# Kernel optimization log

Hardware: AMD Instinct MI355X
Metric: run time of the kernel (lower is better)

Reference implementation:

```python
import jax, jax.numpy as jnp
import numpy as np

B, S, D, H, L, V, NP, GH = 2, 1024, 1024, 16, 6, 32000, 16, 64
DH = D // H
FF = int(D * 4 * 2 / 3)  # SwiGLU hidden = int(dim*ffn_expansion*2/3)


def setup_inputs() -> dict:
    key = jax.random.key(0)
    ks = jax.random.split(key, 12)
    n = lambda k, shp, s=0.02: (jax.random.normal(k, shp, jnp.float32) * s)
    # per-layer memory gate init: -3.0 .. -1.0 across layers
    gate_init = jnp.array([-3.0 + (i / (L - 1)) * 2.0 for i in range(L)], jnp.float32)
    return dict(
        input_ids=jax.random.randint(ks[0], (B, S), 0, V),
        tok_emb=n(ks[1], (V, D)),
        w_init=jnp.zeros((D,), jnp.float32),
        persistent=n(ks[2], (NP, D), 1.0),
        norm1_w=jnp.ones((L, D), jnp.float32),
        norm2_w=jnp.ones((L, D), jnp.float32),
        norm_f_w=jnp.ones((D,), jnp.float32),
        qkv_w=n(ks[3], (L, 3 * D, D)),
        q_norm_w=jnp.ones((L, DH), jnp.float32),
        k_norm_w=jnp.ones((L, DH), jnp.float32),
        gamma_w1=n(ks[4], (L, GH, D)),
        gamma_w2=n(ks[5], (L, 1, GH)),
        memory_gate=gate_init,
        w_o=n(ks[6], (L, D, D), 0.02 / 2 ** 0.5),
        ffn_w1=n(ks[7], (L, FF, D)),
        ffn_w2=n(ks[8], (L, FF, D)),
        ffn_w3=n(ks[9], (L, D, FF)),
    )


def _rms(x, w, eps=1e-6):
    return x * jax.lax.rsqrt(jnp.mean(x * x, axis=-1, keepdims=True) + eps) * w


def _rope_tables():
    inv_freq = 1.0 / (10000.0 ** (jnp.arange(0, DH, 2, dtype=jnp.float32) / DH))
    t = jnp.arange(S, dtype=jnp.float32)
    freqs = jnp.einsum('s,f->sf', t, inv_freq)  # (S, DH/2)
    return jnp.cos(freqs), jnp.sin(freqs)


def _rope(x, cos, sin):  # x: (B,H,S,DH)
    x1, x2 = jnp.split(x, 2, axis=-1)
    return jnp.concatenate([x1 * cos - x2 * sin, x2 * cos + x1 * sin], axis=-1)


def reference(input_ids, tok_emb, w_init, persistent, norm1_w, norm2_w, norm_f_w,
              qkv_w, q_norm_w, k_norm_w, gamma_w1, gamma_w2, memory_gate,
              w_o, ffn_w1, ffn_w2, ffn_w3):
    x = tok_emb[input_ids] + w_init  # (B,S,D)
    cos, sin = _rope_tables()
    causal = jnp.tril(jnp.ones((S, S), dtype=bool))  # True where k <= q
    scale = DH ** -0.5
    # persistent memory: per-head sum of key outer products M_p[h] = sum_j p_jh p_jh^T
    p = persistent.reshape(NP, H, DH)
    Mp = jnp.einsum('nhd,nhe->hde', p, p)
    for i in range(L):
        h = _rms(x, norm1_w[i])
        qkv = h @ qkv_w[i].T  # (B,S,3D)
        q, k, v = jnp.split(qkv, 3, axis=-1)
        q = q.reshape(B, S, H, DH).transpose(0, 2, 1, 3)
        k = k.reshape(B, S, H, DH).transpose(0, 2, 1, 3)
        v = v.reshape(B, S, H, DH).transpose(0, 2, 1, 3)
        q = _rms(q, q_norm_w[i])  # qk_norm
        k = _rms(k, k_norm_w[i])
        q = _rope(q, cos, sin)
        k = _rope(k, cos, sin)
        # gamma gate: Linear -> SiLU -> Linear -> Sigmoid, (B,S,1)
        g = jax.nn.sigmoid(jnp.einsum('oh,bsh->bso', gamma_w2[i],
                                      jax.nn.silu(jnp.einsum('hd,bsd->bsh', gamma_w1[i], h))))
        gk = g[..., 0]  # (B,S)
        # Omega-rule memory: q'_t = (M_p q_t + sum_{i<=t} gamma_i (k_i . q_t) k_i) / (NP + sum_{i<=t} gamma_i)
        mem_scores = jnp.einsum('bhqd,bhkd->bhqk', q, k) * gk[:, None, None, :]
        mem_scores = jnp.where(causal, mem_scores, 0.0)
        mem = jnp.einsum('bhqk,bhkd->bhqd', mem_scores, k)
        mpq = jnp.einsum('hde,bhse->bhsd', Mp, q)
        norm = NP + jnp.cumsum(gk, axis=1)  # (B,S)
        q_proj = (mpq + mem) / norm[:, None, :, None]
        gate = jax.nn.sigmoid(memory_gate[i])
        q = (1 - gate) * q + gate * q_proj
        # causal softmax attention
        attn = jnp.einsum('bhqd,bhkd->bhqk', q, k) * scale
        attn = jnp.where(causal, attn, jnp.finfo(attn.dtype).min)
        pw = jax.nn.softmax(attn, axis=-1)
        o = jnp.einsum('bhqk,bhkd->bhqd', pw, v).transpose(0, 2, 1, 3).reshape(B, S, D)
        x = x + o @ w_o[i].T
        # SwiGLU FFN
        h2 = _rms(x, norm2_w[i])
        x = x + (jax.nn.silu(h2 @ ffn_w1[i].T) * (h2 @ ffn_w2[i].T)) @ ffn_w3[i].T
    x = _rms(x, norm_f_w)
    return x @ tok_emb.T  # tied lm_head, (B,S,V)
```

## Files before the change

kernel.cpp:

```cpp
#include <hip/hip_runtime.h>
#include <hip/hip_bf16.h>
#include <math.h>

#define B 2
#define S 1024
#define D 1024
#define H 16
#define DH 64
#define NL 6
#define GH 64
#define NP 16
#define V 32000
#define FF 2730
#define FFP 2752
#define M (B*S)

typedef float fv4 __attribute__((ext_vector_type(4)));
typedef short bf16x8 __attribute__((ext_vector_type(8)));
typedef unsigned short us4 __attribute__((ext_vector_type(4)));
typedef unsigned short us;

#define MFMA16 __builtin_amdgcn_mfma_f32_16x16x32_bf16
#define G2L16(g, l) __builtin_amdgcn_global_load_lds( \
    (const __attribute__((address_space(1))) void*)(g), \
    (__attribute__((address_space(3))) void*)(l), 16, 0, 0)

__device__ __forceinline__ us f2bf(float f) {
  union { float f; unsigned u; } v; v.f = f;
  unsigned r = v.u + 0x7FFFu + ((v.u >> 16) & 1u);
  return (us)(r >> 16);
}
__device__ __forceinline__ float bf2f(us h) {
  union { unsigned u; float f; } v; v.u = ((unsigned)h) << 16;
  return v.f;
}

template<int N> __device__ __forceinline__ void waitcnt_vm() {
  if constexpr (N == 0)      asm volatile("s_waitcnt vmcnt(0)" ::: "memory");
  else if constexpr (N == 4) asm volatile("s_waitcnt vmcnt(4)" ::: "memory");
  else if constexpr (N == 8) asm volatile("s_waitcnt vmcnt(8)" ::: "memory");
  else if constexpr (N == 6) asm volatile("s_waitcnt vmcnt(6)" ::: "memory");
}

__device__ __forceinline__ int xcd_remap(int flat, int nwg) {
  int q = nwg >> 3, r = nwg & 7;
  int xcd = flat & 7, idx = flat >> 3;
  return (xcd < r) ? (xcd * (q + 1) + idx) : (r * (q + 1) + (xcd - r) * q + idx);
}

__global__ __launch_bounds__(256) void k_embed(const int* __restrict__ ids,
                                               const float* __restrict__ emb,
                                               const float* __restrict__ winit,
                                               float* __restrict__ x) {
  int m = blockIdx.x, t = threadIdx.x;
  int id = ids[m];
  fv4 a = *(const fv4*)(emb + (size_t)id * D + 4*t);
  fv4 w = *(const fv4*)(winit + 4*t);
  *(fv4*)(x + (size_t)m * D + 4*t) = a + w;
}

__global__ void k_rope_tables(float* __restrict__ cosT, float* __restrict__ sinT) {
  int idx = blockIdx.x * blockDim.x + threadIdx.x;
  if (idx >= S * 32) return;
  int s = idx >> 5, f = idx & 31;
  float inv = powf(10000.0f, -2.0f * (float)f / (float)DH);
  float ang = (float)s * inv;
  cosT[idx] = cosf(ang);
  sinT[idx] = sinf(ang);
}

__global__ __launch_bounds__(256) void k_mp(const float* __restrict__ pers,
                                            us* __restrict__ Mp) {
  int h = blockIdx.x, t = threadIdx.x;
  __shared__ float p[NP][DH];
  for (int i = t; i < NP * DH; i += 256) {
    int n = i / DH, dh = i % DH;
    p[n][dh] = pers[(size_t)n * D + h * DH + dh];
  }
  __syncthreads();
  for (int i = t; i < DH * DH; i += 256) {
    int d = i / DH, e = i % DH;
    float s = 0.f;
#pragma unroll
    for (int n = 0; n < NP; n++) s += p[n][d] * p[n][e];
    Mp[(size_t)h * DH * DH + i] = f2bf(s);
  }
}

__global__ __launch_bounds__(256) void k_rms(const float* __restrict__ in,
                                             const float* __restrict__ w,
                                             us* __restrict__ outb) {
  int m = blockIdx.x, t = threadIdx.x;
  fv4 v = *(const fv4*)(in + (size_t)m * D + 4*t);
  float ss = v[0]*v[0] + v[1]*v[1] + v[2]*v[2] + v[3]*v[3];
#pragma unroll
  for (int off = 32; off > 0; off >>= 1) ss += __shfl_down(ss, off);
  __shared__ float buf[4];
  if ((t & 63) == 0) buf[t >> 6] = ss;
  __syncthreads();
  float tot = buf[0] + buf[1] + buf[2] + buf[3];
  float r = rsqrtf(tot * (1.0f / (float)D) + 1e-6f);
  fv4 wv = *(const fv4*)(w + 4*t);
  fv4 res = v * r * wv;
  us4 o; o[0]=f2bf(res[0]); o[1]=f2bf(res[1]); o[2]=f2bf(res[2]); o[3]=f2bf(res[3]);
  *(us4*)(outb + (size_t)m * D + 4*t) = o;
}

__global__ __launch_bounds__(256) void k_rmsg(const float* __restrict__ in,
                                              const float* __restrict__ w,
                                              const float* __restrict__ w1,
                                              const float* __restrict__ w2,
                                              us* __restrict__ outb,
                                              float* __restrict__ gko) {
  int m = blockIdx.x, t = threadIdx.x;
  __shared__ float hrow[D];
  __shared__ float buf[4];
  __shared__ float part[4][64];
  fv4 v = *(const fv4*)(in + (size_t)m * D + 4*t);
  float ss = v[0]*v[0] + v[1]*v[1] + v[2]*v[2] + v[3]*v[3];
#pragma unroll
  for (int off = 32; off > 0; off >>= 1) ss += __shfl_down(ss, off);
  if ((t & 63) == 0) buf[t >> 6] = ss;
  __syncthreads();
  float tot = buf[0] + buf[1] + buf[2] + buf[3];
  float r = rsqrtf(tot * (1.0f / (float)D) + 1e-6f);
  fv4 wv = *(const fv4*)(w + 4*t);
  fv4 res = v * r * wv;
  us4 o; o[0]=f2bf(res[0]); o[1]=f2bf(res[1]); o[2]=f2bf(res[2]); o[3]=f2bf(res[3]);
  *(us4*)(outb + (size_t)m * D + 4*t) = o;
  *(fv4*)&hrow[4*t] = res;
  __syncthreads();
  int oo = t & 63, seg = t >> 6;
  const float* wr = w1 + (size_t)oo * D + seg * 256;
  const float* hr = hrow + seg * 256;
  float acc = 0.f;
  for (int j = 0; j < 256; j += 4) {
    fv4 wv4 = *(const fv4*)(wr + j);
    acc += wv4[0]*hr[j] + wv4[1]*hr[j+1] + wv4[2]*hr[j+2] + wv4[3]*hr[j+3];
  }
  part[seg][oo] = acc;
  __syncthreads();
  if (t < 64) {
    float dot = part[0][t] + part[1][t] + part[2][t] + part[3][t];
    float sv = dot / (1.f + expf(-dot));
    float val = sv * w2[t];
#pragma unroll
    for (int off = 32; off > 0; off >>= 1) val += __shfl_down(val, off);
    if (t == 0) gko[m] = 1.f / (1.f + expf(-val));
  }
}

__global__ __launch_bounds__(256) void k_cvt(const float* __restrict__ src,
                                             us* __restrict__ dst, int n) {
  for (size_t i = ((size_t)blockIdx.x * 256 + threadIdx.x) * 4; i < (size_t)n;
       i += (size_t)gridDim.x * 1024) {
    fv4 v = *(const fv4*)(src + i);
    us4 o; o[0]=f2bf(v[0]); o[1]=f2bf(v[1]); o[2]=f2bf(v[2]); o[3]=f2bf(v[3]);
    *(us4*)(dst + i) = o;
  }
}

#define CVT_N1 786432
#define CVT_N2 262144
#define CVT_N3 698880
#define CVT_N4 698880
#define CVT_N5 704512
__global__ __launch_bounds__(256) void k_cvtw(const float* __restrict__ s1,
                                              const float* __restrict__ s2,
                                              const float* __restrict__ s3,
                                              const float* __restrict__ s4,
                                              const float* __restrict__ s5,
                                              us* __restrict__ d1, us* __restrict__ d2,
                                              us* __restrict__ d3, us* __restrict__ d4,
                                              us* __restrict__ d5) {
  const int TOT = CVT_N1 + CVT_N2 + CVT_N3 + CVT_N4 + CVT_N5;
  for (int i = blockIdx.x * 256 + threadIdx.x; i < TOT; i += gridDim.x * 256) {
    const float* s; us* d; int j = i;
    if (j < CVT_N1) { s = s1; d = d1; }
    else if ((j -= CVT_N1) < CVT_N2) { s = s2; d = d2; }
    else if ((j -= CVT_N2) < CVT_N3) { s = s3; d = d3; }
    else if ((j -= CVT_N3) < CVT_N4) { s = s4; d = d4; }
    else {
      j -= CVT_N4;
      int r = j / (FFP/4), c = (j % (FFP/4)) * 4;
      us4 o;
#pragma unroll
      for (int q = 0; q < 4; q++) {
        int cc = c + q;
        o[q] = (cc < FF) ? f2bf(s5[(size_t)r * FF + cc]) : (us)0;
      }
      *(us4*)&d5[(size_t)r * FFP + c] = o;
      continue;
    }
    fv4 v = *(const fv4*)(s + (size_t)4 * j);
    us4 o; o[0]=f2bf(v[0]); o[1]=f2bf(v[1]); o[2]=f2bf(v[2]); o[3]=f2bf(v[3]);
    *(us4*)&d[(size_t)4 * j] = o;
  }
}

template<int ACW, int BCW>
__device__ __forceinline__ void pg_stage(const us* __restrict__ A,
                                         const us* __restrict__ W,
                                         us* bufA, us* bufB,
                                         int m0, int n0, int Nn, int Kk,
                                         int tile, int w, int lane, int lr, int sx) {
#pragma unroll
  for (int i = 0; i < ACW; i++) {
    int chunk = w * ACW + i;
    G2L16(A + (size_t)(m0 + chunk*8 + lr) * Kk + tile*64 + sx, bufA + chunk*512 + lane*8);
  }
#pragma unroll
  for (int i = 0; i < BCW; i++) {
    int chunk = w * BCW + i;
    int wrow = n0 + chunk*8 + lr;
    if (wrow >= Nn) wrow = Nn - 1;
    G2L16(W + (size_t)wrow * Kk + tile*64 + sx, bufB + chunk*512 + lane*8);
  }
}

template<int EPI, int BM, int BN>
__global__ __launch_bounds__(256) void k_pgemm(const us* __restrict__ A,
                                               const us* __restrict__ W,
                                               float* __restrict__ C,
                                               int Nn, int Kk) {
  constexpr int FM = BM / 32, FN = BN / 32;
  constexpr int ACW = BM / 32, BCW = BN / 32;
  constexpr int L = ACW + BCW;
  __shared__ __attribute__((aligned(16))) us lds[2][(BM + BN) * 64];
  int t = threadIdx.x, lane = t & 63, w = t >> 6;
  int l16 = lane & 15, lkb = lane >> 4, lr = lane >> 3;
  int sx = ((lane & 7) ^ lr) * 8;
  int sw = l16 & 7;
  int gx = gridDim.x, nwg = gx * gridDim.y;
  int nf = xcd_remap(blockIdx.y * gx + blockIdx.x, nwg);
  int m0 = (nf % gx) * BM, n0 = (nf / gx) * BN;
  int wr = w >> 1, wc = w & 1;
  int NK = Kk >> 6;

  pg_stage<ACW,BCW>(A, W, lds[0], lds[0] + BM*64, m0, n0, Nn, Kk, 0, w, lane, lr, sx);
  pg_stage<ACW,BCW>(A, W, lds[1], lds[1] + BM*64, m0, n0, Nn, Kk, 1, w, lane, lr, sx);

  fv4 acc[FM][FN] = {};
  for (int T = 0; T < NK; T++) {
    if (T == NK - 1) waitcnt_vm<0>(); else waitcnt_vm<L>();
    __builtin_amdgcn_s_barrier();
    const us* bufA = lds[T & 1];
    const us* bufB = bufA + BM*64;
    bf16x8 af[2][FM], bfh[2][FN];
#pragma unroll
    for (int kk = 0; kk < 2; kk++) {
#pragma unroll
      for (int i = 0; i < FM; i++)
        af[kk][i] = *(const bf16x8*)&bufA[(wr*(BM/2) + i*16 + l16)*64 + (((kk*4+lkb)) ^ sw)*8];
#pragma unroll
      for (int j = 0; j < FN; j++)
        bfh[kk][j] = *(const bf16x8*)&bufB[(wc*(BN/2) + j*16 + l16)*64 + (((kk*4+lkb)) ^ sw)*8];
    }
    __builtin_amdgcn_s_barrier();
    if (T + 2 < NK)
      pg_stage<ACW,BCW>(A, W, lds[T & 1], lds[T & 1] + BM*64, m0, n0, Nn, Kk, T + 2, w, lane, lr, sx);
    __builtin_amdgcn_s_setprio(1);
#pragma unroll
    for (int kk = 0; kk < 2; kk++)
#pragma unroll
      for (int i = 0; i < FM; i++)
#pragma unroll
        for (int j = 0; j < FN; j++)
          acc[i][j] = MFMA16(af[kk][i], bfh[kk][j], acc[i][j], 0, 0, 0);
    __builtin_amdgcn_s_setprio(0);
  }

#pragma unroll
  for (int i = 0; i < FM; i++) {
    int gr0 = m0 + wr*(BM/2) + i*16 + lkb*4;
#pragma unroll
    for (int j = 0; j < FN; j++) {
      int gc = n0 + wc*(BN/2) + j*16 + l16;
      if (gc < Nn) {
#pragma unroll
        for (int r = 0; r < 4; r++) {
          size_t idx = (size_t)(gr0 + r) * Nn + gc;
          float val = acc[i][j][r];
          if (EPI == 0) C[idx] = val;
          else C[idx] += val;
        }
      }
    }
  }
}

__device__ __forceinline__ void pf_stage(const us* __restrict__ A,
                                         const us* __restrict__ W1,
                                         const us* __restrict__ W2,
                                         us* buf, int m0, int n0, int Nn, int Kk,
                                         int tile, int w, int lane, int lr, int sx) {
#pragma unroll
  for (int i = 0; i < 4; i++) {
    int chunk = w * 4 + i;
    G2L16(A + (size_t)(m0 + chunk*8 + lr) * Kk + tile*64 + sx, buf + chunk*512 + lane*8);
  }
#pragma unroll
  for (int i = 0; i < 2; i++) {
    int chunk = w * 2 + i;
    int wrow = n0 + chunk*8 + lr;
    if (wrow >= Nn) wrow = Nn - 1;
    G2L16(W1 + (size_t)wrow * Kk + tile*64 + sx, buf + 8192 + chunk*512 + lane*8);
    G2L16(W2 + (size_t)wrow * Kk + tile*64 + sx, buf + 12288 + chunk*512 + lane*8);
  }
}

__global__ __launch_bounds__(256) void k_pffn12(const us* __restrict__ A,
                                                const us* __restrict__ W1,
                                                const us* __restrict__ W2,
                                                us* __restrict__ Cb,
                                                int Nn, int Kk) {
  __shared__ __attribute__((aligned(16))) us lds[2][16384];
  int t = threadIdx.x, lane = t & 63, w = t >> 6;
  int l16 = lane & 15, lkb = lane >> 4, lr = lane >> 3;
  int sx = ((lane & 7) ^ lr) * 8;
  int sw = l16 & 7;
  int gx = gridDim.x, nwg = gx * gridDim.y;
  int nf = xcd_remap(blockIdx.y * gx + blockIdx.x, nwg);
  int m0 = (nf % gx) * 128, n0 = (nf / gx) * 64;
  int wr = w >> 1, wc = w & 1;
  int NK = Kk >> 6;

  pf_stage(A, W1, W2, lds[0], m0, n0, Nn, Kk, 0, w, lane, lr, sx);
  pf_stage(A, W1, W2, lds[1], m0, n0, Nn, Kk, 1, w, lane, lr, sx);

  fv4 acc1[4][2] = {}, acc2[4][2] = {};
  for (int T = 0; T < NK; T++) {
    if (T == NK - 1) waitcnt_vm<0>(); else waitcnt_vm<8>();
    __builtin_amdgcn_s_barrier();
    const us* buf = lds[T & 1];
    bf16x8 af[2][4], b1f[2][2], b2f[2][2];
#pragma unroll
    for (int kk = 0; kk < 2; kk++) {
#pragma unroll
      for (int i = 0; i < 4; i++)
        af[kk][i] = *(const bf16x8*)&buf[(wr*64 + i*16 + l16)*64 + ((kk*4+lkb) ^ sw)*8];
#pragma unroll
      for (int j = 0; j < 2; j++) {
        b1f[kk][j] = *(const bf16x8*)&buf[8192  + (wc*32 + j*16 + l16)*64 + ((kk*4+lkb) ^ sw)*8];
        b2f[kk][j] = *(const bf16x8*)&buf[12288 + (wc*32 + j*16 + l16)*64 + ((kk*4+lkb) ^ sw)*8];
      }
    }
    __builtin_amdgcn_s_barrier();
    if (T + 2 < NK)
      pf_stage(A, W1, W2, lds[T & 1], m0, n0, Nn, Kk, T + 2, w, lane, lr, sx);
    __builtin_amdgcn_s_setprio(1);
#pragma unroll
    for (int kk = 0; kk < 2; kk++)
#pragma unroll
      for (int i = 0; i < 4; i++)
#pragma unroll
        for (int j = 0; j < 2; j++) {
          acc1[i][j] = MFMA16(af[kk][i], b1f[kk][j], acc1[i][j], 0, 0, 0);
          acc2[i][j] = MFMA16(af[kk][i], b2f[kk][j], acc2[i][j], 0, 0, 0);
        }
    __builtin_amdgcn_s_setprio(0);
  }

#pragma unroll
  for (int i = 0; i < 4; i++) {
    int gr0 = m0 + wr*64 + i*16 + lkb*4;
#pragma unroll
    for (int j = 0; j < 2; j++) {
      int gc = n0 + wc*32 + j*16 + l16;
      if (gc < Nn) {
#pragma unroll
        for (int r = 0; r < 4; r++) {
          float v1 = acc1[i][j][r], v2 = acc2[i][j][r];
          float sv = v1 / (1.f + expf(-v1));
          Cb[(size_t)(gr0 + r) * FFP + gc] = f2bf(sv * v2);
        }
      }
    }
  }
}

__global__ __launch_bounds__(256) void k_pqkv(const us* __restrict__ A,
                                              const us* __restrict__ W,
                                              const float* __restrict__ qnw,
                                              const float* __restrict__ knw,
                                              const float* __restrict__ cosT,
                                              const float* __restrict__ sinT,
                                              us* __restrict__ qb,
                                              us* __restrict__ kb,
                                              us* __restrict__ vb) {
  const int Kk = D, Nn = 3 * D;
  __shared__ __attribute__((aligned(16))) us lds[2][16384];
  int t = threadIdx.x, lane = t & 63, w = t >> 6;
  int l16 = lane & 15, lkb = lane >> 4, lr = lane >> 3;
  int sx = ((lane & 7) ^ lr) * 8;
  int sw = l16 & 7;
  int gx = gridDim.x, nwg = gx * gridDim.y;
  int nf = xcd_remap(blockIdx.y * gx + blockIdx.x, nwg);
  int m0 = (nf % gx) * 128, n0 = (nf / gx) * 128;
  int wr = w >> 1, wc = w & 1;
  int NK = Kk >> 6;

  pg_stage<4,4>(A, W, lds[0], lds[0] + 8192, m0, n0, Nn, Kk, 0, w, lane, lr, sx);
  pg_stage<4,4>(A, W, lds[1], lds[1] + 8192, m0, n0, Nn, Kk, 1, w, lane, lr, sx);

  fv4 acc[4][4] = {};
  for (int T = 0; T < NK; T++) {
    if (T == NK - 1) waitcnt_vm<0>(); else waitcnt_vm<8>();
    __builtin_amdgcn_s_barrier();
    const us* bufA = lds[T & 1];
    const us* bufB = bufA + 8192;
    bf16x8 af[2][4], bfh[2][4];
#pragma unroll
    for (int kk = 0; kk < 2; kk++) {
#pragma unroll
      for (int i = 0; i < 4; i++) {
        af[kk][i]  = *(const bf16x8*)&bufA[(wr*64 + i*16 + l16)*64 + ((kk*4+lkb) ^ sw)*8];
        bfh[kk][i] = *(const bf16x8*)&bufB[(wc*64 + i*16 + l16)*64 + ((kk*4+lkb) ^ sw)*8];
      }
    }
    __builtin_amdgcn_s_barrier();
    if (T + 2 < NK)
      pg_stage<4,4>(A, W, lds[T & 1], lds[T & 1] + 8192, m0, n0, Nn, Kk, T + 2, w, lane, lr, sx);
    __builtin_amdgcn_s_setprio(1);
#pragma unroll
    for (int kk = 0; kk < 2; kk++)
#pragma unroll
      for (int i = 0; i < 4; i++)
#pragma unroll
        for (int j = 0; j < 4; j++)
          acc[i][j] = MFMA16(af[kk][i], bfh[kk][j], acc[i][j], 0, 0, 0);
    __builtin_amdgcn_s_setprio(0);
  }

  int part = n0 >> 10;
  int hd = ((n0 & 1023) + wc * 64) >> 6;
  us* dst = (part == 0) ? qb : ((part == 1) ? kb : vb);
  if (part == 2) {
#pragma unroll
    for (int i = 0; i < 4; i++)
#pragma unroll
      for (int r = 0; r < 4; r++) {
        int m = m0 + wr*64 + i*16 + lkb*4 + r;
        int b = m >> 10, s = m & 1023;
        us* drow = dst + (((size_t)(b*H + hd)) * S + s) * 64;
#pragma unroll
        for (int j = 0; j < 4; j++) drow[j*16 + l16] = f2bf(acc[i][j][r]);
      }
  } else {
    const float* nw = (part == 0) ? qnw : knw;
    float w0 = nw[l16], w1 = nw[16 + l16], w2 = nw[32 + l16], w3 = nw[48 + l16];
#pragma unroll
    for (int i = 0; i < 4; i++)
#pragma unroll
      for (int r = 0; r < 4; r++) {
        int m = m0 + wr*64 + i*16 + lkb*4 + r;
        int b = m >> 10, s = m & 1023;
        float a0 = acc[i][0][r], a1 = acc[i][1][r], a2 = acc[i][2][r], a3 = acc[i][3][r];
        float s2 = a0*a0 + a1*a1 + a2*a2 + a3*a3;
        s2 += __shfl_xor(s2, 1); s2 += __shfl_xor(s2, 2);
        s2 += __shfl_xor(s2, 4); s2 += __shfl_xor(s2, 8);
        float rs = rsqrtf(s2 * (1.0f / (float)DH) + 1e-6f);
        float v0 = a0 * rs * w0, v1 = a1 * rs * w1, v2 = a2 * rs * w2, v3 = a3 * rs * w3;
        float c0 = cosT[s*32 + l16],      sn0 = sinT[s*32 + l16];
        float c1 = cosT[s*32 + 16 + l16], sn1 = sinT[s*32 + 16 + l16];
        us* drow = dst + (((size_t)(b*H + hd)) * S + s) * 64;
        drow[l16]      = f2bf(v0 * c0 - v2 * sn0);
        drow[16 + l16] = f2bf(v1 * c1 - v3 * sn1);
        drow[32 + l16] = f2bf(v2 * c0 + v0 * sn0);
        drow[48 + l16] = f2bf(v3 * c1 + v1 * sn1);
      }
  }
}

struct G8 { const us* A; const us* W; int K; int m0; int n0; };

__device__ __forceinline__ void g8_issue(const G8& g, us* lds8, int q, int t) {
  int tile = q >> 2, h = q & 3;
  us* buf = lds8 + (size_t)(tile & 1) * 32768;
  const us* Gp = (h < 2) ? g.A : g.W;
  int rbase = ((h < 2) ? g.m0 : g.n0) + (h & 1) * 128;
  us* part = buf + (h >> 1) * 16384 + (h & 1) * 8192;
  int r8 = t >> 3;
  int sl = (((t & 7) ^ (r8 & 7)) * 8);
#pragma unroll
  for (int c = 0; c < 2; c++) {
    const us* src = Gp + (size_t)(rbase + c * 64 + r8) * g.K + tile * 64 + sl;
    us* dst = part + c * 4096 + t * 8;
    G2L16(src, dst);
  }
}

__global__ __launch_bounds__(512, 2) void k_gemm8(const us* __restrict__ A,
                                                  const us* __restrict__ W,
                                                  float* __restrict__ C,
                                                  int Nn, int Kk) {
  __shared__ __attribute__((aligned(16))) us lds8[65536];
  int t = threadIdx.x, lane = t & 63, w = t >> 6;
  int wm = w >> 2, wn = w & 3;
  int l16 = lane & 15, lkb = lane >> 4;
  int gx = gridDim.x, nwg = gx * gridDim.y;
  int nf = xcd_remap(blockIdx.y * gx + blockIdx.x, nwg);
  int m0 = (nf % gx) * 256, n0 = (nf / gx) * 256;
  G8 g{A, W, Kk, m0, n0};
  int NK = Kk >> 6, QMAX = NK * 4;

  int q = 0;
  for (; q < 7 && q < QMAX; ++q) g8_issue(g, lds8, q, t);

  fv4 acc[8][4] = {};
  int arow = wm * 128 + l16;
  int brow = wn * 64 + l16;
  int sw = l16 & 7;

  for (int T = 0; T < NK; ++T) {
    if (q < QMAX) { g8_issue(g, lds8, q, t); q++; }
    if (T == NK - 1) asm volatile("s_waitcnt vmcnt(0)" ::: "memory");
    else             asm volatile("s_waitcnt vmcnt(8)" ::: "memory");
    __builtin_amdgcn_s_barrier();
    const us* buf = lds8 + (size_t)(T & 1) * 32768;
    bf16x8 a0[8], a1[8], b0[4], b1[4];
#pragma unroll
    for (int i = 0; i < 8; i++) {
      a0[i] = *(const bf16x8*)&buf[(arow + i*16)*64 + ((lkb     ) ^ sw)*8];
      a1[i] = *(const bf16x8*)&buf[(arow + i*16)*64 + ((lkb +  4) ^ sw)*8];
    }
#pragma unroll
    for (int j = 0; j < 4; j++) {
      b0[j] = *(const bf16x8*)&buf[16384 + (brow + j*16)*64 + ((lkb    ) ^ sw)*8];
      b1[j] = *(const bf16x8*)&buf[16384 + (brow + j*16)*64 + ((lkb + 4) ^ sw)*8];
    }
    __builtin_amdgcn_s_barrier();
    __builtin_amdgcn_s_setprio(1);
#pragma unroll
    for (int i = 0; i < 8; i++)
#pragma unroll
      for (int j = 0; j < 4; j++)
        acc[i][j] = MFMA16(a0[i], b0[j], acc[i][j], 0, 0, 0);
    __builtin_amdgcn_s_setprio(0);
    if (q < QMAX) { g8_issue(g, lds8, q, t); q++; }
    if (q < QMAX) { g8_issue(g, lds8, q, t); q++; }
    if (q < QMAX) { g8_issue(g, lds8, q, t); q++; }
    __builtin_amdgcn_s_setprio(1);
#pragma unroll
    for (int i = 0; i < 8; i++)
#pragma unroll
      for (int j = 0; j < 4; j++)
        acc[i][j] = MFMA16(a1[i], b1[j], acc[i][j], 0, 0, 0);
    __builtin_amdgcn_s_setprio(0);
  }

#pragma unroll
  for (int i = 0; i < 8; i++) {
    int gr0 = m0 + wm*128 + i*16 + lkb*4;
#pragma unroll
    for (int j = 0; j < 4; j++) {
      int gc = n0 + wn*64 + j*16 + l16;
#pragma unroll
      for (int r = 0; r < 4; r++)
        C[(size_t)(gr0 + r) * Nn + gc] = acc[i][j][r];
    }
  }
}

__global__ __launch_bounds__(256) void k_tr2(const us* __restrict__ ksrc,
                                             const us* __restrict__ vsrc,
                                             us* __restrict__ kdst,
                                             us* __restrict__ vdst) {
  __shared__ __attribute__((aligned(16))) us tile[64*72];
  int st = blockIdx.x, bh = blockIdx.y, t = threadIdx.x;
  const us* src = blockIdx.z ? vsrc : ksrc;
  us* dst = blockIdx.z ? vdst : kdst;
  const us* sp = src + ((size_t)bh * S + st*64) * 64;
#pragma unroll
  for (int p = 0; p < 2; p++) {
    int idx = t + p*256;
    int r = idx >> 3, c = (idx & 7)*8;
    *(bf16x8*)&tile[r*72 + c] = *(const bf16x8*)&sp[(size_t)idx*8];
  }
  __syncthreads();
  int d = t >> 2;
#pragma unroll
  for (int cc = 0; cc < 16; cc += 8) {
    int s0 = (t & 3)*16 + cc;
    bf16x8 vv;
#pragma unroll
    for (int j2 = 0; j2 < 8; j2++) vv[j2] = (short)tile[(s0+j2)*72 + d];
    *(bf16x8*)&dst[((size_t)bh*64 + d)*S + st*64 + s0] = vv;
  }
}

__global__ __launch_bounds__(1024) void k_cumsum(const float* __restrict__ gk,
                                                 float* __restrict__ nrm) {
  int b = blockIdx.x, t = threadIdx.x;
  int lane = t & 63, wv = t >> 6;
  float s = gk[b*S + t];
#pragma unroll
  for (int off = 1; off < 64; off <<= 1) {
    float y = __shfl_up(s, off, 64);
    if (lane >= off) s += y;
  }
  __shared__ float wsum[16];
  if (lane == 63) wsum[wv] = s;
  __syncthreads();
  if (t < 16) {
    float v = wsum[t];
    float sv = v;
#pragma unroll
    for (int off = 1; off < 16; off <<= 1) {
      float y = __shfl_up(sv, off, 16);
      if (t >= off) sv += y;
    }
    wsum[t] = sv - v;
  }
  __syncthreads();
  nrm[b*S + t] = (float)NP + s + wsum[wv];
}

#define SM_OFF 24.0f
__global__ __launch_bounds__(256) void k_matt(const us* __restrict__ qb,
                                              const us* __restrict__ kb,
                                              const us* __restrict__ kbT,
                                              const us* __restrict__ vbT,
                                              const us* __restrict__ MpB,
                                              const float* __restrict__ gk,
                                              const float* __restrict__ nrm,
                                              const float* __restrict__ mg, int layer,
                                              us* __restrict__ ob) {
  int nf = xcd_remap(blockIdx.y * 8 + blockIdx.x, 256);
  int xx = nf & 7, bh = nf >> 3;
  int b = bh >> 4, hh = bh & 15;
  int t = threadIdx.x, lane = t & 63, w = t >> 6;
  int l16 = lane & 15, lg = lane >> 4;

  __shared__ __attribute__((aligned(16))) us Qs[64*72];
  __shared__ __attribute__((aligned(16))) us Ks[64*72];
  __shared__ __attribute__((aligned(16))) us Ts[64*72];
  __shared__ __attribute__((aligned(16))) us Ps[64*72];
  __shared__ float gks_[64], nrms[64];

  float gate = 1.f / (1.f + expf(-mg[layer]));

  for (int sel = 0; sel < 2; sel++) {
    int qt = sel ? (15 - xx) : xx;
    __syncthreads();

    {
      const us* src = qb + ((size_t)bh * S + qt*64) * 64;
      const us* mp = MpB + (size_t)hh * 4096;
#pragma unroll
      for (int p = 0; p < 2; p++) {
        int idx = t + p*256;
        int r = idx >> 3, c = (idx & 7) * 8;
        *(bf16x8*)&Qs[r*72 + c] = *(const bf16x8*)&src[(size_t)idx*8];
        *(bf16x8*)&Ts[r*72 + c] = *(const bf16x8*)&mp[(size_t)idx*8];
      }
      if (t < 64) nrms[t] = nrm[b*S + qt*64 + t];
    }
    __syncthreads();

    bf16x8 aq0 = *(const bf16x8*)&Qs[(16*w + l16)*72 + lg*8];
    bf16x8 aq1 = *(const bf16x8*)&Qs[(16*w + l16)*72 + 32 + lg*8];

    fv4 am[4];
#pragma unroll
    for (int j = 0; j < 4; j++) {
      bf16x8 b0 = *(const bf16x8*)&Ts[(16*j + l16)*72 + lg*8];
      bf16x8 b1 = *(const bf16x8*)&Ts[(16*j + l16)*72 + 32 + lg*8];
      fv4 z = {};
      z = MFMA16(aq0, b0, z, 0, 0, 0);
      z = MFMA16(aq1, b1, z, 0, 0, 0);
      am[j] = z;
    }

    for (int kt = 0; kt <= qt; kt++) {
      __syncthreads();
      {
        const us* ksrc = kb + ((size_t)bh * S + kt*64) * 64;
#pragma unroll
        for (int p = 0; p < 2; p++) {
          int idx = t + p*256;
          int r = idx >> 3, c = (idx & 7) * 8;
          *(bf16x8*)&Ks[r*72 + c] = *(const bf16x8*)&ksrc[(size_t)idx*8];
        }
        int d = t >> 2, c0 = (t & 3) * 16;
        const us* tsrc = kbT + ((size_t)bh*64 + d) * S + kt*64 + c0;
        *(bf16x8*)&Ts[d*72 + c0]     = *(const bf16x8*)&tsrc[0];
        *(bf16x8*)&Ts[d*72 + c0 + 8] = *(const bf16x8*)&tsrc[8];
        if (t < 64) gks_[t] = gk[b*S + kt*64 + t];
      }
      __syncthreads();
      fv4 sc[4];
#pragma unroll
      for (int j = 0; j < 4; j++) {
        bf16x8 b0 = *(const bf16x8*)&Ks[(16*j + l16)*72 + lg*8];
        bf16x8 b1 = *(const bf16x8*)&Ks[(16*j + l16)*72 + 32 + lg*8];
        fv4 z = {};
        z = MFMA16(aq0, b0, z, 0, 0, 0);
        z = MFMA16(aq1, b1, z, 0, 0, 0);
        sc[j] = z;
      }
      if (kt < qt) {
#pragma unroll
        for (int j = 0; j < 4; j++) {
          float g = gks_[16*j + l16];
#pragma unroll
          for (int r = 0; r < 4; r++)
            Ps[(16*w + lg*4 + r)*72 + 16*j + l16] = f2bf(sc[j][r] * g);
        }
      } else {
#pragma unroll
        for (int j = 0; j < 4; j++) {
          int kj = 16*j + l16;
          float g = gks_[kj];
#pragma unroll
          for (int r = 0; r < 4; r++) {
            int qi = 16*w + lg*4 + r;
            Ps[qi*72 + kj] = (kj > qi) ? (us)0 : f2bf(sc[j][r] * g);
          }
        }
      }
      bf16x8 ap0 = *(const bf16x8*)&Ps[(16*w + l16)*72 + lg*8];
      bf16x8 ap1 = *(const bf16x8*)&Ps[(16*w + l16)*72 + 32 + lg*8];
#pragma unroll
      for (int j = 0; j < 4; j++) {
        bf16x8 b0 = *(const bf16x8*)&Ts[(16*j + l16)*72 + lg*8];
        bf16x8 b1 = *(const bf16x8*)&Ts[(16*j + l16)*72 + 32 + lg*8];
        am[j] = MFMA16(ap0, b0, am[j], 0, 0, 0);
        am[j] = MFMA16(ap1, b1, am[j], 0, 0, 0);
      }
    }

#pragma unroll
    for (int j = 0; j < 4; j++)
#pragma unroll
      for (int r = 0; r < 4; r++) {
        int qi = 16*w + lg*4 + r, dj = 16*j + l16;
        float qold = bf2f(Qs[qi*72 + dj]);
        float qn = (1.f - gate) * qold + gate * (am[j][r] / nrms[qi]);
        Qs[qi*72 + dj] = f2bf(qn);
      }
    aq0 = *(const bf16x8*)&Qs[(16*w + l16)*72 + lg*8];
    aq1 = *(const bf16x8*)&Qs[(16*w + l16)*72 + 32 + lg*8];

    float lsum[4] = {};
    fv4 ao[4] = {};
    for (int kt = 0; kt <= qt; kt++) {
      __syncthreads();
      {
        const us* ksrc = kb + ((size_t)bh * S + kt*64) * 64;
#pragma unroll
        for (int p = 0; p < 2; p++) {
          int idx = t + p*256;
          int r = idx >> 3, c = (idx & 7) * 8;
          *(bf16x8*)&Ks[r*72 + c] = *(const bf16x8*)&ksrc[(size_t)idx*8];
        }
        int d = t >> 2, c0 = (t & 3) * 16;
        const us* tsrc = vbT + ((size_t)bh*64 + d) * S + kt*64 + c0;
        *(bf16x8*)&Ts[d*72 + c0]     = *(const bf16x8*)&tsrc[0];
        *(bf16x8*)&Ts[d*72 + c0 + 8] = *(const bf16x8*)&tsrc[8];
      }
      __syncthreads();
      fv4 sc[4];
#pragma unroll
      for (int j = 0; j < 4; j++) {
        bf16x8 b0 = *(const bf16x8*)&Ks[(16*j + l16)*72 + lg*8];
        bf16x8 b1 = *(const bf16x8*)&Ks[(16*j + l16)*72 + 32 + lg*8];
        fv4 z = {};
        z = MFMA16(aq0, b0, z, 0, 0, 0);
        z = MFMA16(aq1, b1, z, 0, 0, 0);
        sc[j] = z;
      }
      if (kt < qt) {
#pragma unroll
        for (int j = 0; j < 4; j++)
#pragma unroll
          for (int r = 0; r < 4; r++) {
            float p = __expf(fmaf(sc[j][r], 0.125f, -SM_OFF));
            lsum[r] += p;
            Ps[(16*w + lg*4 + r)*72 + 16*j + l16] = f2bf(p);
          }
      } else {
#pragma unroll
        for (int j = 0; j < 4; j++) {
          int kj = 16*j + l16;
#pragma unroll
          for (int r = 0; r < 4; r++) {
            int qi = 16*w + lg*4 + r;
            float p = (kj > qi) ? 0.f : __expf(fmaf(sc[j][r], 0.125f, -SM_OFF));
            lsum[r] += p;
            Ps[qi*72 + kj] = f2bf(p);
          }
        }
      }
      bf16x8 ap0 = *(const bf16x8*)&Ps[(16*w + l16)*72 + lg*8];
      bf16x8 ap1 = *(const bf16x8*)&Ps[(16*w + l16)*72 + 32 + lg*8];
#pragma unroll
      for (int j = 0; j < 4; j++) {
        bf16x8 b0 = *(const bf16x8*)&Ts[(16*j + l16)*72 + lg*8];
        bf16x8 b1 = *(const bf16x8*)&Ts[(16*j + l16)*72 + 32 + lg*8];
        ao[j] = MFMA16(ap0, b0, ao[j], 0, 0, 0);
        ao[j] = MFMA16(ap1, b1, ao[j], 0, 0, 0);
      }
    }

#pragma unroll
    for (int r = 0; r < 4; r++) {
      float l = lsum[r];
      l += __shfl_xor(l, 1);
      l += __shfl_xor(l, 2);
      l += __shfl_xor(l, 4);
      l += __shfl_xor(l, 8);
      lsum[r] = l;
    }
#pragma unroll
    for (int j = 0; j < 4; j++)
#pragma unroll
      for (int r = 0; r < 4; r++) {
        int qi = 16*w + lg*4 + r;
        ob[((size_t)b*S + qt*64 + qi) * D + hh*64 + 16*j + l16] = f2bf(ao[j][r] / lsum[r]);
      }
  }
}

extern "C" void kernel_launch(void* const* d_in, const int* in_sizes, int n_in,
                              void* d_out, int out_size, void* d_ws, size_t ws_size,
                              hipStream_t stream) {
  const int*   ids      = (const int*)d_in[0];
  const float* tok_emb  = (const float*)d_in[1];
  const float* w_init   = (const float*)d_in[2];
  const float* persist  = (const float*)d_in[3];
  const float* norm1_w  = (const float*)d_in[4];
  const float* norm2_w  = (const float*)d_in[5];
  const float* norm_f_w = (const float*)d_in[6];
  const float* qkv_w    = (const float*)d_in[7];
  const float* q_norm_w = (const float*)d_in[8];
  const float* k_norm_w = (const float*)d_in[9];
  const float* gamma_w1 = (const float*)d_in[10];
  const float* gamma_w2 = (const float*)d_in[11];
  const float* mem_gate = (const float*)d_in[12];
  const float* w_o      = (const float*)d_in[13];
  const float* ffn_w1   = (const float*)d_in[14];
  const float* ffn_w2   = (const float*)d_in[15];
  const float* ffn_w3   = (const float*)d_in[16];
  float* out = (float*)d_out;

  float* ws   = (float*)d_ws;
  float* x    = ws;
  us*    hbf  = (us*)(x + 2097152);
  float* gk   = x + 2097152 + 1048576;
  float* nrm  = gk + 2048;
  float* cosT = nrm + 2048;
  float* sinT = cosT + 32768;
  us*    MpBH = (us*)(sinT + 32768);
  float* h    = sinT + 32768 + 65536;
  float* qkv  = h + 2097152;
  us*    obf  = (us*)(qkv + 6291456);
  us*    qb   = obf + 2097152;
  us*    kb   = qb + 2097152;
  us*    vb   = kb + 2097152;
  us*    kbT  = vb + 2097152;
  us*    vbT  = kbT + 2097152;
  us*    f1bf = vbT + 2097152;
  us*    wq   = f1bf + (size_t)M*FFP;
  us*    wo   = wq + 3145728;
  us*    w1c  = wo + 1048576;
  us*    w2c  = w1c + 2795520;
  us*    w3c  = w2c + 2795520;
  us*    temb = (us*)h;

  k_embed<<<M, 256, 0, stream>>>(ids, tok_emb, w_init, x);
  k_rope_tables<<<(S*32 + 255)/256, 256, 0, stream>>>(cosT, sinT);
  k_mp<<<H, 256, 0, stream>>>(persist, MpBH);

  for (int l = 0; l < NL; l++) {
    k_cvtw<<<2048, 256, 0, stream>>>(qkv_w + (size_t)l*3*D*D, w_o + (size_t)l*D*D,
                                     ffn_w1 + (size_t)l*FF*D, ffn_w2 + (size_t)l*FF*D,
                                     ffn_w3 + (size_t)l*D*FF,
                                     wq, wo, w1c, w2c, w3c);
    k_rmsg<<<M, 256, 0, stream>>>(x, norm1_w + (size_t)l * D,
                                  gamma_w1 + (size_t)l*GH*D, gamma_w2 + (size_t)l*GH,
                                  hbf, gk);
    k_pqkv<<<dim3(16, 24), 256, 0, stream>>>(hbf, wq,
                                             q_norm_w + (size_t)l*DH, k_norm_w + (size_t)l*DH,
                                             cosT, sinT, qb, kb, vb);
    k_tr2<<<dim3(S/64, B*H, 2), 256, 0, stream>>>(kb, vb, kbT, vbT);
    k_cumsum<<<B, S, 0, stream>>>(gk, nrm);
    k_matt<<<dim3(8, B*H), 256, 0, stream>>>(qb, kb, kbT, vbT, MpBH, gk, nrm, mem_gate, l, obf);
    k_pgemm<2,64,64><<<dim3(M/64, D/64), 256, 0, stream>>>(obf, wo, x, D, D);
    k_rms<<<M, 256, 0, stream>>>(x, norm2_w + (size_t)l * D, hbf);
    k_pffn12<<<dim3(M/128, (FF+63)/64), 256, 0, stream>>>(hbf, w1c, w2c, f1bf, FF, D);
    k_pgemm<2,64,64><<<dim3(M/64, D/64), 256, 0, stream>>>(f1bf, w3c, x, D, FFP);
  }

  k_rms<<<M, 256, 0, stream>>>(x, norm_f_w, hbf);
  k_cvt<<<2048, 256, 0, stream>>>(tok_emb, temb, V*D);
  k_gemm8<<<dim3(8, V/256), 512, 0, stream>>>(hbf, temb, out, V, D);
}
```

Before: 1.501 ms.

## Double-buffer K/V tiles in memory-attention kernel with async global-to-LDS loads

Rewrites the K/V tile staging in the fused memory+softmax attention kernel. Tiles now go straight from global memory to LDS through global_load_lds into a two-stage buffer with XOR-swizzled layout, and the next tiles are prefetched while the current one is computed. Fragments are read into registers between barriers, and MFMA blocks get raised wave priority. The gate vector is preloaded once and the Mp matrix is staged once per block. This aims to hide load latency and cut synchronisation in the attention loop, at the cost of more LDS and registers and the risk of waitcnt or barrier ordering errors.

```diff
diff --git a/kernel.cpp b/kernel.cpp
--- a/kernel.cpp
+++ b/kernel.cpp
@@ -617,6 +617,16 @@
 }
 
 #define SM_OFF 24.0f
+
+__device__ __forceinline__ void m_stage(const us* __restrict__ src, int rstride,
+                                        us* buf, int w, int lane, int lr, int sx8) {
+#pragma unroll
+  for (int i = 0; i < 2; i++) {
+    int rbase = i * 32 + w * 8;
+    G2L16(src + (size_t)(rbase + lr) * rstride + sx8, buf + rbase * 64 + lane * 8);
+  }
+}
+
 __global__ __launch_bounds__(256) void k_matt(const us* __restrict__ qb,
                                               const us* __restrict__ kb,
                                               const us* __restrict__ kbT,
@@ -630,29 +640,43 @@
   int xx = nf & 7, bh = nf >> 3;
   int b = bh >> 4, hh = bh & 15;
   int t = threadIdx.x, lane = t & 63, w = t >> 6;
-  int l16 = lane & 15, lg = lane >> 4;
+  int l16 = lane & 15, lg = lane >> 4, lr = lane >> 3;
+  int sx8 = ((lane & 7) ^ lr) * 8;
+  int sw = l16 & 7;
 
   __shared__ __attribute__((aligned(16))) us Qs[64*72];
-  __shared__ __attribute__((aligned(16))) us Ks[64*72];
-  __shared__ __attribute__((aligned(16))) us Ts[64*72];
+  __shared__ __attribute__((aligned(16))) us Ms[64*72];
   __shared__ __attribute__((aligned(16))) us Ps[64*72];
-  __shared__ float gks_[64], nrms[64];
+  __shared__ __attribute__((aligned(16))) us KT[2][2][64*64];
+  __shared__ float gkL[S], nrms[64];
 
   float gate = 1.f / (1.f + expf(-mg[layer]));
+  const us* kbB = kb + (size_t)bh * S * 64;
+  const us* ktB = kbT + (size_t)bh * 64 * S;
+  const us* vtB = vbT + (size_t)bh * 64 * S;
+
+  {
+    const us* mp = MpB + (size_t)hh * 4096;
+#pragma unroll
+    for (int p = 0; p < 2; p++) {
+      int idx = t + p*256;
+      int r = idx >> 3, c = (idx & 7) * 8;
+      *(bf16x8*)&Ms[r*72 + c] = *(const bf16x8*)&mp[(size_t)idx*8];
+    }
+#pragma unroll
+    for (int p = 0; p < 4; p++) gkL[t + p*256] = gk[b*S + t + p*256];
+  }
 
   for (int sel = 0; sel < 2; sel++) {
     int qt = sel ? (15 - xx) : xx;
     __syncthreads();
-
     {
       const us* src = qb + ((size_t)bh * S + qt*64) * 64;
-      const us* mp = MpB + (size_t)hh * 4096;
 #pragma unroll
       for (int p = 0; p < 2; p++) {
         int idx = t + p*256;
         int r = idx >> 3, c = (idx & 7) * 8;
         *(bf16x8*)&Qs[r*72 + c] = *(const bf16x8*)&src[(size_t)idx*8];
-        *(bf16x8*)&Ts[r*72 + c] = *(const bf16x8*)&mp[(size_t)idx*8];
       }
       if (t < 64) nrms[t] = nrm[b*S + qt*64 + t];
     }
@@ -664,70 +688,76 @@
     fv4 am[4];
 #pragma unroll
     for (int j = 0; j < 4; j++) {
-      bf16x8 b0 = *(const bf16x8*)&Ts[(16*j + l16)*72 + lg*8];
-      bf16x8 b1 = *(const bf16x8*)&Ts[(16*j + l16)*72 + 32 + lg*8];
+      bf16x8 b0 = *(const bf16x8*)&Ms[(16*j + l16)*72 + lg*8];
+      bf16x8 b1 = *(const bf16x8*)&Ms[(16*j + l16)*72 + 32 + lg*8];
       fv4 z = {};
       z = MFMA16(aq0, b0, z, 0, 0, 0);
       z = MFMA16(aq1, b1, z, 0, 0, 0);
       am[j] = z;
     }
 
+    m_stage(kbB,            64, KT[0][0], w, lane, lr, sx8);
+    m_stage(ktB,            S,  KT[0][1], w, lane, lr, sx8);
+    m_stage(kbB + 4096,     64, KT[1][0], w, lane, lr, sx8);
+    m_stage(ktB + 64,       S,  KT[1][1], w, lane, lr, sx8);
     for (int kt = 0; kt <= qt; kt++) {
-      __syncthreads();
-      {
-        const us* ksrc = kb + ((size_t)bh * S + kt*64) * 64;
-#pragma unroll
-        for (int p = 0; p < 2; p++) {
-          int idx = t + p*256;
-          int r = idx >> 3, c = (idx & 7) * 8;
-          *(bf16x8*)&Ks[r*72 + c] = *(const bf16x8*)&ksrc[(size_t)idx*8];
-        }
-        int d = t >> 2, c0 = (t & 3) * 16;
-        const us* tsrc = kbT + ((size_t)bh*64 + d) * S + kt*64 + c0;
-        *(bf16x8*)&Ts[d*72 + c0]     = *(const bf16x8*)&tsrc[0];
-        *(bf16x8*)&Ts[d*72 + c0 + 8] = *(const bf16x8*)&tsrc[8];
-        if (t < 64) gks_[t] = gk[b*S + kt*64 + t];
-      }
-      __syncthreads();
+      int ks = kt * 64;
+      if (kt == qt) waitcnt_vm<0>(); else waitcnt_vm<4>();
+      __builtin_amdgcn_s_barrier();
+      const us* bK = KT[kt & 1][0];
+      const us* bT = KT[kt & 1][1];
+      bf16x8 kf0[4], kf1[4], tf0[4], tf1[4];
+      float gv[4];
+#pragma unroll
+      for (int j = 0; j < 4; j++) {
+        int row = 16*j + l16;
+        kf0[j] = *(const bf16x8*)&bK[row*64 + ((lg    ) ^ sw)*8];
+        kf1[j] = *(const bf16x8*)&bK[row*64 + ((lg + 4) ^ sw)*8];
+        tf0[j] = *(const bf16x8*)&bT[row*64 + ((lg    ) ^ sw)*8];
+        tf1[j] = *(const bf16x8*)&bT[row*64 + ((lg + 4) ^ sw)*8];
+        gv[j] = gkL[ks + row];
+      }
+      __builtin_amdgcn_s_barrier();
+      if (kt + 2 <= qt) {
+        m_stage(kbB + (size_t)(kt+2)*4096, 64, KT[kt & 1][0], w, lane, lr, sx8);
+        m_stage(ktB + (kt+2)*64,           S,  KT[kt & 1][1], w, lane, lr, sx8);
+      }
       fv4 sc[4];
+      __builtin_amdgcn_s_setprio(1);
 #pragma unroll
       for (int j = 0; j < 4; j++) {
-        bf16x8 b0 = *(const bf16x8*)&Ks[(16*j + l16)*72 + lg*8];
-        bf16x8 b1 = *(const bf16x8*)&Ks[(16*j + l16)*72 + 32 + lg*8];
         fv4 z = {};
-        z = MFMA16(aq0, b0, z, 0, 0, 0);
-        z = MFMA16(aq1, b1, z, 0, 0, 0);
+        z = MFMA16(aq0, kf0[j], z, 0, 0, 0);
+        z = MFMA16(aq1, kf1[j], z, 0, 0, 0);
         sc[j] = z;
       }
+      __builtin_amdgcn_s_setprio(0);
       if (kt < qt) {
 #pragma unroll
-        for (int j = 0; j < 4; j++) {
-          float g = gks_[16*j + l16];
+        for (int j = 0; j < 4; j++)
 #pragma unroll
           for (int r = 0; r < 4; r++)
-            Ps[(16*w + lg*4 + r)*72 + 16*j + l16] = f2bf(sc[j][r] * g);
-        }
+            Ps[(16*w + lg*4 + r)*72 + 16*j + l16] = f2bf(sc[j][r] * gv[j]);
       } else {
 #pragma unroll
         for (int j = 0; j < 4; j++) {
           int kj = 16*j + l16;
-          float g = gks_[kj];
 #pragma unroll
           for (int r = 0; r < 4; r++) {
             int qi = 16*w + lg*4 + r;
-            Ps[qi*72 + kj] = (kj > qi) ? (us)0 : f2bf(sc[j][r] * g);
+            Ps[qi*72 + kj] = (kj > qi) ? (us)0 : f2bf(sc[j][r] * gv[j]);
           }
         }
       }
       bf16x8 ap0 = *(const bf16x8*)&Ps[(16*w + l16)*72 + lg*8];
       bf16x8 ap1 = *(const bf16x8*)&Ps[(16*w + l16)*72 + 32 + lg*8];
+      __builtin_amdgcn_s_setprio(1);
 #pragma unroll
       for (int j = 0; j < 4; j++) {
-        bf16x8 b0 = *(const bf16x8*)&Ts[(16*j + l16)*72 + lg*8];
-        bf16x8 b1 = *(const bf16x8*)&Ts[(16*j + l16)*72 + 32 + lg*8];
-        am[j] = MFMA16(ap0, b0, am[j], 0, 0, 0);
-        am[j] = MFMA16(ap1, b1, am[j], 0, 0, 0);
-      }
+        am[j] = MFMA16(ap0, tf0[j], am[j], 0, 0, 0);
+        am[j] = MFMA16(ap1, tf1[j], am[j], 0, 0, 0);
+      }
+      __builtin_amdgcn_s_setprio(0);
     }
 
 #pragma unroll
@@ -744,32 +774,39 @@
 
     float lsum[4] = {};
     fv4 ao[4] = {};
+    m_stage(kbB,            64, KT[0][0], w, lane, lr, sx8);
+    m_stage(vtB,            S,  KT[0][1], w, lane, lr, sx8);
+    m_stage(kbB + 4096,     64, KT[1][0], w, lane, lr, sx8);
+    m_stage(vtB + 64,       S,  KT[1][1], w, lane, lr, sx8);
     for (int kt = 0; kt <= qt; kt++) {
-      __syncthreads();
-      {
-        const us* ksrc = kb + ((size_t)bh * S + kt*64) * 64;
-#pragma unroll
-        for (int p = 0; p < 2; p++) {
-          int idx = t + p*256;
-          int r = idx >> 3, c = (idx & 7) * 8;
-          *(bf16x8*)&Ks[r*72 + c] = *(const bf16x8*)&ksrc[(size_t)idx*8];
-        }
-        int d = t >> 2, c0 = (t & 3) * 16;
-        const us* tsrc = vbT + ((size_t)bh*64 + d) * S + kt*64 + c0;
-        *(bf16x8*)&Ts[d*72 + c0]     = *(const bf16x8*)&tsrc[0];
-        *(bf16x8*)&Ts[d*72 + c0 + 8] = *(const bf16x8*)&tsrc[8];
-      }
-      __syncthreads();
+      if (kt == qt) waitcnt_vm<0>(); else waitcnt_vm<4>();
+      __builtin_amdgcn_s_barrier();
+      const us* bK = KT[kt & 1][0];
+      const us* bV = KT[kt & 1][1];
+      bf16x8 kf0[4], kf1[4], vf0[4], vf1[4];
+#pragma unroll
+      for (int j = 0; j < 4; j++) {
+        int row = 16*j + l16;
+        kf0[j] = *(const bf16x8*)&bK[row*64 + ((lg    ) ^ sw)*8];
+        kf1[j] = *(const bf16x8*)&bK[row*64 + ((lg + 4) ^ sw)*8];
+        vf0[j] = *(const bf16x8*)&bV[row*64 + ((lg    ) ^ sw)*8];
+        vf1[j] = *(const bf16x8*)&bV[row*64 + ((lg + 4) ^ sw)*8];
+      }
+      __builtin_amdgcn_s_barrier();
+      if (kt + 2 <= qt) {
+        m_stage(kbB + (size_t)(kt+2)*4096, 64, KT[kt & 1][0], w, lane, lr, sx8);
+        m_stage(vtB + (kt+2)*64,           S,  KT[kt & 1][1], w, lane, lr, sx8);
+      }
       fv4 sc[4];
+      __builtin_amdgcn_s_setprio(1);
 #pragma unroll
       for (int j = 0; j < 4; j++) {
-        bf16x8 b0 = *(const bf16x8*)&Ks[(16*j + l16)*72 + lg*8];
-        bf16x8 b1 = *(const bf16x8*)&Ks[(16*j + l16)*72 + 32 + lg*8];
         fv4 z = {};
-        z = MFMA16(aq0, b0, z, 0, 0, 0);
-        z = MFMA16(aq1, b1, z, 0, 0, 0);
+        z = MFMA16(aq0, kf0[j], z, 0, 0, 0);
+        z = MFMA16(aq1, kf1[j], z, 0, 0, 0);
         sc[j] = z;
       }
+      __builtin_amdgcn_s_setprio(0);
       if (kt < qt) {
 #pragma unroll
         for (int j = 0; j < 4; j++)
@@ -794,13 +831,13 @@
       }
       bf16x8 ap0 = *(const bf16x8*)&Ps[(16*w + l16)*72 + lg*8];
       bf16x8 ap1 = *(const bf16x8*)&Ps[(16*w + l16)*72 + 32 + lg*8];
+      __builtin_amdgcn_s_setprio(1);
 #pragma unroll
       for (int j = 0; j < 4; j++) {
-        bf16x8 b0 = *(const bf16x8*)&Ts[(16*j + l16)*72 + lg*8];
-        bf16x8 b1 = *(const bf16x8*)&Ts[(16*j + l16)*72 + 32 + lg*8];
-        ao[j] = MFMA16(ap0, b0, ao[j], 0, 0, 0);
-        ao[j] = MFMA16(ap1, b1, ao[j], 0, 0, 0);
-      }
+        ao[j] = MFMA16(ap0, vf0[j], ao[j], 0, 0, 0);
+        ao[j] = MFMA16(ap1, vf1[j], ao[j], 0, 0, 0);
+      }
+      __builtin_amdgcn_s_setprio(0);
     }
 
 #pragma unroll
```

Measured after the change: 1.432 ms. 4.6% less time.
